# Performance work log

Hardware: AMD Instinct MI355X
Metric: run time of the kernel (lower is better)

## Reference

```python
import jax, jax.numpy as jnp
import numpy as np

EPS = 1e-6
TEMPERATURE = 1.0


def setup_inputs() -> dict:
    key = jax.random.key(0)
    ks = jax.random.split(key, 8)
    B, N, T, H, NH = 128, 16, 32, 128, 4
    L = (N + 1) * T
    node_enc = jax.random.normal(ks[0], (B, T, H), dtype=jnp.float32)
    neigh_enc = jax.random.normal(ks[1], (B, N, T, H), dtype=jnp.float32)
    attn_mask = jax.random.randint(ks[2], (B, L), 0, 2).astype(bool)
    attn_mask = attn_mask.at[:, 0].set(False)  # ensure no fully-masked row
    w_qs = jax.random.normal(ks[3], (NH, H, H), dtype=jnp.float32) * 0.05
    w_ks = jax.random.normal(ks[4], (NH, H, H), dtype=jnp.float32) * 0.05
    w_vs = jax.random.normal(ks[5], (NH, H, H), dtype=jnp.float32) * 0.05
    prj_w = jax.random.normal(ks[6], (H, NH * H), dtype=jnp.float32) * 0.05
    prj_b = jnp.zeros((H,), dtype=jnp.float32)
    ln_gamma = jnp.ones((H,), dtype=jnp.float32)
    ln_beta = jnp.zeros((H,), dtype=jnp.float32)
    return {"node_enc": node_enc, "neigh_enc": neigh_enc, "attn_mask": attn_mask,
            "current_time_step": 5, "w_qs": w_qs, "w_ks": w_ks, "w_vs": w_vs,
            "prj_w": prj_w, "prj_b": prj_b, "ln_gamma": ln_gamma, "ln_beta": ln_beta}


def reference(node_enc, neigh_enc, attn_mask, current_time_step,
              w_qs, w_ks, w_vs, prj_w, prj_b, ln_gamma, ln_beta):
    B, T, H = node_enc.shape
    N = neigh_enc.shape[1]
    NH = w_qs.shape[0]
    q = node_enc[:, current_time_step]                       # [B, H]
    # split(neigh_enc,1,dim=1) + cat(dim=2) == reshape to [B, N*T, H]
    kv = jnp.concatenate([node_enc, neigh_enc.reshape(B, N * T, H)], axis=1)  # [B, L, H]
    q_s = jnp.einsum('bh,nhd->nbd', q, w_qs)                 # [NH, B, H]
    k_s = jnp.einsum('blh,nhd->nbld', kv, w_ks)              # [NH, B, L, H]
    v_s = jnp.einsum('blh,nhd->nbld', kv, w_vs)              # [NH, B, L, H]
    S = jnp.einsum('nbd,nbld->nbl', q_s, k_s)                # [NH, B, L]
    S = jnp.where(attn_mask[None, :, :], -jnp.inf, S)
    S = S / (TEMPERATURE * jnp.sqrt(jnp.float32(H)))
    A = jax.nn.softmax(S, axis=-1)                           # [NH, B, L]
    ctx = jnp.einsum('nbl,nbld->nbd', A, v_s)                # [NH, B, H]
    # torch cat of head-splits along dim=-1 -> [B, NH*H], head-major
    cat = jnp.transpose(ctx, (1, 0, 2)).reshape(B, NH * H)
    proj = cat @ prj_w.T + prj_b                             # [B, H]
    x = proj + q
    mean = jnp.mean(x, axis=-1, keepdims=True)
    var = jnp.var(x, axis=-1, keepdims=True)
    out = (x - mean) / jnp.sqrt(var + EPS) * ln_gamma + ln_beta
    slf_attn = jnp.sum(A, axis=0)[:, None, :]                # [B, 1, L]
    return (out, slf_attn)
```

## Files before the change

kernel.cpp:

```cpp
#include <hip/hip_runtime.h>

#define B_  128
#define N_  16
#define T_  32
#define H_  128
#define NH_ 4
#define L_  544
#define CH  64
#define NC  9

__global__ __launch_bounds__(256) void qk_kernel(
    const float* __restrict__ node_enc, const int* __restrict__ cts_p,
    const float* __restrict__ w_qs, const float* __restrict__ w_ks,
    float* __restrict__ qk_ws)
{
    const int blk = blockIdx.x;
    const int b = blk & 127, n = blk >> 7;
    const int t = threadIdx.x;
    __shared__ float q_sh[H_];
    __shared__ float ps[256];
    __shared__ float qs_sh[H_];

    if (t < H_) q_sh[t] = node_enc[(size_t)b*T_*H_ + cts_p[0]*H_ + t];
    __syncthreads();
    {
        int d = t & 127, half = t >> 7;
        const float* w  = w_qs + (size_t)n*H_*H_ + (half*64)*H_ + d;
        const float* qh = q_sh + half*64;
        float acc = 0.f;
        #pragma unroll 8
        for (int h = 0; h < 64; ++h) acc += qh[h] * w[h*H_];
        ps[t] = acc;
    }
    __syncthreads();
    if (t < H_) qs_sh[t] = ps[t] + ps[t+128];
    __syncthreads();
    {
        int h = t & 127, half = t >> 7;
        const float4* w  = (const float4*)(w_ks + (size_t)n*H_*H_ + h*H_ + half*64);
        const float4* qs = (const float4*)(qs_sh + half*64);
        float acc = 0.f;
        #pragma unroll
        for (int i = 0; i < 16; ++i) {
            float4 wv = w[i], qv = qs[i];
            acc += wv.x*qv.x + wv.y*qv.y + wv.z*qv.z + wv.w*qv.w;
        }
        ps[t] = acc;
    }
    __syncthreads();
    if (t < H_) qk_ws[(b*NH_ + n)*H_ + t] = ps[t] + ps[t+128];
}

__global__ __launch_bounds__(256) void attn_main_kernel(
    const float* __restrict__ node_enc, const float* __restrict__ neigh_enc,
    const int* __restrict__ attn_mask, const float* __restrict__ qk_ws,
    float* __restrict__ S_ws, float* __restrict__ wpart_ws,
    float* __restrict__ stats_ws)
{
    const int blk = blockIdx.x;
    const int b = blk / NC, c = blk % NC;
    const int t = threadIdx.x;
    const int l0 = c * CH;
    const int R  = min(CH, L_ - l0);

    __shared__ __align__(16) float kv_sh[CH*132];
    __shared__ __align__(16) float qk_sh[4*132];
    __shared__ float S_sh[CH*5];
    __shared__ float P_sh[CH*6];
    __shared__ int   msk_sh[CH];

    for (int j = t; j < 4*H_; j += 256) {
        int g = j >> 7, h = j & 127;
        qk_sh[g*132 + h] = qk_ws[(b*NH_ + g)*H_ + h];
    }
    if (t < R) msk_sh[t] = attn_mask[b*L_ + l0 + t];
    for (int j = t; j < R*32; j += 256) {
        int r = j >> 5, cc = j & 31;
        int l = l0 + r;
        const float* rowp = (l < T_)
            ? node_enc  + (size_t)b*T_*H_ + l*H_
            : neigh_enc + (size_t)b*N_*T_*H_ + (size_t)(l - T_)*H_;
        float4 v = ((const float4*)rowp)[cc];
        *((float4*)(kv_sh + r*132 + cc*4)) = v;
    }
    __syncthreads();

    {
        int r = t >> 2, g = t & 3;
        float S = -INFINITY;
        if (r < R) {
            const float4* kvv = (const float4*)(kv_sh + r*132);
            const float4* qv  = (const float4*)(qk_sh + g*132);
            float acc = 0.f;
            #pragma unroll
            for (int i = 0; i < 32; ++i) {
                float4 a = kvv[i], q = qv[i];
                acc += a.x*q.x + a.y*q.y + a.z*q.z + a.w*q.w;
            }
            S = msk_sh[r] ? -INFINITY : acc * 0.08838834764831845f;
            S_ws[((size_t)b*L_ + l0 + r)*NH_ + g] = S;
        }
        S_sh[r*5 + g] = S;
    }
    __syncthreads();

    {
        int w = t >> 6, lane = t & 63;
        float v = S_sh[lane*5 + w];
        float m = v;
        #pragma unroll
        for (int off = 32; off > 0; off >>= 1) m = fmaxf(m, __shfl_xor(m, off, 64));
        m = fmaxf(m, -1e30f);
        float p = __expf(v - m);
        P_sh[lane*6 + w] = p;
        float s = p;
        #pragma unroll
        for (int off = 32; off > 0; off >>= 1) s += __shfl_xor(s, off, 64);
        if (lane == 0) {
            stats_ws[((b*NC + c)*NH_ + w)*2 + 0] = m;
            stats_ws[((b*NC + c)*NH_ + w)*2 + 1] = s;
        }
    }
    __syncthreads();

    {
        int h = t & 127, gp = t >> 7;
        float acc0 = 0.f, acc1 = 0.f;
        #pragma unroll 4
        for (int r = 0; r < R; ++r) {
            float  kvv = kv_sh[r*132 + h];
            float2 p = *((const float2*)(P_sh + r*6 + gp*2));
            acc0 += p.x * kvv;
            acc1 += p.y * kvv;
        }
        float* wp = wpart_ws + (size_t)(b*NC + c)*NH_*H_;
        wp[(gp*2+0)*H_ + h] = acc0;
        wp[(gp*2+1)*H_ + h] = acc1;
    }
}

__global__ __launch_bounds__(512) void finish_kernel(
    const float* __restrict__ node_enc, const int* __restrict__ cts_p,
    const float* __restrict__ w_vs, const float* __restrict__ prj_w,
    const float* __restrict__ prj_b, const float* __restrict__ ln_gamma,
    const float* __restrict__ ln_beta, const float* __restrict__ S_ws,
    const float* __restrict__ wpart_ws, const float* __restrict__ stats_ws,
    float* __restrict__ d_out)
{
    const int b = blockIdx.x, t = threadIdx.x;
    __shared__ float stats_sh[NC*NH_*2];
    __shared__ float m_sh[NH_], inv_sh[NH_];
    __shared__ float scale_sh[NC*NH_];
    __shared__ __align__(16) float wctx_sh[NH_*H_];
    __shared__ __align__(16) float cat_sh[NH_*H_];
    __shared__ float part_sh[512];
    __shared__ float x_sh[H_];
    __shared__ float st2[2];

    if (t < NC*NH_*2) stats_sh[t] = stats_ws[b*NC*NH_*2 + t];
    __syncthreads();
    if (t < NH_) {
        float m = -INFINITY;
        #pragma unroll
        for (int c = 0; c < NC; ++c) m = fmaxf(m, stats_sh[(c*NH_+t)*2]);
        float s = 0.f;
        #pragma unroll
        for (int c = 0; c < NC; ++c)
            s += stats_sh[(c*NH_+t)*2+1] * __expf(stats_sh[(c*NH_+t)*2] - m);
        m_sh[t] = m;
        inv_sh[t] = 1.0f / s;
    }
    __syncthreads();
    if (t < NC*NH_) {
        int c = t >> 2, n = t & 3;
        scale_sh[t] = __expf(stats_sh[(c*NH_+n)*2] - m_sh[n]) * inv_sh[n];
    }
    __syncthreads();

    {
        float m0 = m_sh[0], m1 = m_sh[1], m2 = m_sh[2], m3 = m_sh[3];
        float i0 = inv_sh[0], i1 = inv_sh[1], i2 = inv_sh[2], i3 = inv_sh[3];
        float* slf = d_out + B_*H_ + b*L_;
        const float4* Sr = (const float4*)(S_ws + (size_t)b*L_*NH_);
        for (int l = t; l < L_; l += 512) {
            float4 s4 = Sr[l];
            slf[l] = __expf(s4.x - m0)*i0 + __expf(s4.y - m1)*i1
                   + __expf(s4.z - m2)*i2 + __expf(s4.w - m3)*i3;
        }
    }
    {
        int n = t >> 7;
        const float* wp = wpart_ws + (size_t)b*NC*NH_*H_;
        float acc = 0.f;
        #pragma unroll
        for (int c = 0; c < NC; ++c)
            acc += wp[c*NH_*H_ + t] * scale_sh[c*NH_ + n];
        wctx_sh[t] = acc;
    }
    __syncthreads();
    {
        int n = t >> 7, d = t & 127;
        const float* w  = w_vs + (size_t)n*H_*H_ + d;
        const float* wc = wctx_sh + n*H_;
        float acc = 0.f;
        #pragma unroll 8
        for (int h = 0; h < H_; ++h) acc += wc[h] * w[h*H_];
        cat_sh[t] = acc;
    }
    __syncthreads();
    {
        int j = t >> 2, q = t & 3;
        const float4* w  = (const float4*)(prj_w + (size_t)j*(NH_*H_) + q*128);
        const float4* cc = (const float4*)(cat_sh + q*128);
        float acc = 0.f;
        #pragma unroll
        for (int i = 0; i < 32; ++i) {
            float4 wv = w[i], cv = cc[i];
            acc += wv.x*cv.x + wv.y*cv.y + wv.z*cv.z + wv.w*cv.w;
        }
        part_sh[t] = acc;
    }
    __syncthreads();
    if (t < H_) {
        float x = part_sh[4*t] + part_sh[4*t+1] + part_sh[4*t+2] + part_sh[4*t+3]
                + prj_b[t] + node_enc[(size_t)b*T_*H_ + cts_p[0]*H_ + t];
        x_sh[t] = x;
    }
    __syncthreads();
    if (t < 64) {
        float v0 = x_sh[t], v1 = x_sh[t+64];
        float s1 = v0 + v1, s2 = v0*v0 + v1*v1;
        #pragma unroll
        for (int off = 32; off > 0; off >>= 1) {
            s1 += __shfl_xor(s1, off, 64);
            s2 += __shfl_xor(s2, off, 64);
        }
        if (t == 0) {
            float mean = s1 / (float)H_;
            float var  = s2 / (float)H_ - mean*mean;
            st2[0] = mean;
            st2[1] = rsqrtf(var + 1e-6f);
        }
    }
    __syncthreads();
    if (t < H_)
        d_out[b*H_ + t] = (x_sh[t] - st2[0]) * st2[1] * ln_gamma[t] + ln_beta[t];
}

extern "C" void kernel_launch(void* const* d_in, const int* in_sizes, int n_in,
                              void* d_out, int out_size, void* d_ws, size_t ws_size,
                              hipStream_t stream) {
    const float* node_enc  = (const float*)d_in[0];
    const float* neigh_enc = (const float*)d_in[1];
    const int*   attn_mask = (const int*)d_in[2];
    const int*   cts       = (const int*)d_in[3];
    const float* w_qs      = (const float*)d_in[4];
    const float* w_ks      = (const float*)d_in[5];
    const float* w_vs      = (const float*)d_in[6];
    const float* prj_w     = (const float*)d_in[7];
    const float* prj_b     = (const float*)d_in[8];
    const float* ln_gamma  = (const float*)d_in[9];
    const float* ln_beta   = (const float*)d_in[10];

    float* qk_ws    = (float*)d_ws;
    float* S_ws     = qk_ws + (size_t)B_*NH_*H_;
    float* wpart_ws = S_ws + (size_t)B_*L_*NH_;
    float* stats_ws = wpart_ws + (size_t)B_*NC*NH_*H_;

    qk_kernel<<<B_*NH_, 256, 0, stream>>>(node_enc, cts, w_qs, w_ks, qk_ws);
    attn_main_kernel<<<B_*NC, 256, 0, stream>>>(node_enc, neigh_enc, attn_mask,
                                                qk_ws, S_ws, wpart_ws, stats_ws);
    finish_kernel<<<B_, 512, 0, stream>>>(node_enc, cts, w_vs, prj_w, prj_b,
                                          ln_gamma, ln_beta, S_ws, wpart_ws,
                                          stats_ws, (float*)d_out);
}
```

Baseline: 129.7 us.

## Store chunk-local softmax probs, split finish kernel into two roles, coalesce projection

The attention kernel now writes chunk-local exponentiated probabilities instead of raw scores, so the finish kernel rescales them by per-chunk factors instead of recomputing four exps per position. The finish kernel launches two blocks per batch: one writes the summed attention map, the other does the context, value and projection path plus layernorm. The output projection is rewritten so each wavefront reads contiguous prj_w rows and reduces with shuffles, giving coalesced loads. A launch-bounds occupancy hint is added to the main kernel. The cost is duplicated stats loading in both role blocks.

```diff
diff --git a/kernel.cpp b/kernel.cpp
--- a/kernel.cpp
+++ b/kernel.cpp
@@ -51,10 +51,10 @@
     if (t < H_) qk_ws[(b*NH_ + n)*H_ + t] = ps[t] + ps[t+128];
 }
 
-__global__ __launch_bounds__(256) void attn_main_kernel(
+__global__ __launch_bounds__(256, 4) void attn_main_kernel(
     const float* __restrict__ node_enc, const float* __restrict__ neigh_enc,
     const int* __restrict__ attn_mask, const float* __restrict__ qk_ws,
-    float* __restrict__ S_ws, float* __restrict__ wpart_ws,
+    float* __restrict__ P_ws, float* __restrict__ wpart_ws,
     float* __restrict__ stats_ws)
 {
     const int blk = blockIdx.x;
@@ -98,7 +98,6 @@
                 acc += a.x*q.x + a.y*q.y + a.z*q.z + a.w*q.w;
             }
             S = msk_sh[r] ? -INFINITY : acc * 0.08838834764831845f;
-            S_ws[((size_t)b*L_ + l0 + r)*NH_ + g] = S;
         }
         S_sh[r*5 + g] = S;
     }
@@ -122,6 +121,11 @@
         }
     }
     __syncthreads();
+
+    for (int j = t; j < R*NH_; j += 256) {
+        int r = j >> 2, g = j & 3;
+        P_ws[((size_t)b*L_ + l0 + r)*NH_ + g] = P_sh[r*6 + g];
+    }
 
     {
         int h = t & 127, gp = t >> 7;
@@ -143,19 +147,15 @@
     const float* __restrict__ node_enc, const int* __restrict__ cts_p,
     const float* __restrict__ w_vs, const float* __restrict__ prj_w,
     const float* __restrict__ prj_b, const float* __restrict__ ln_gamma,
-    const float* __restrict__ ln_beta, const float* __restrict__ S_ws,
+    const float* __restrict__ ln_beta, const float* __restrict__ P_ws,
     const float* __restrict__ wpart_ws, const float* __restrict__ stats_ws,
     float* __restrict__ d_out)
 {
-    const int b = blockIdx.x, t = threadIdx.x;
+    const int b = blockIdx.x >> 1, role = blockIdx.x & 1;
+    const int t = threadIdx.x;
     __shared__ float stats_sh[NC*NH_*2];
     __shared__ float m_sh[NH_], inv_sh[NH_];
     __shared__ float scale_sh[NC*NH_];
-    __shared__ __align__(16) float wctx_sh[NH_*H_];
-    __shared__ __align__(16) float cat_sh[NH_*H_];
-    __shared__ float part_sh[512];
-    __shared__ float x_sh[H_];
-    __shared__ float st2[2];
 
     if (t < NC*NH_*2) stats_sh[t] = stats_ws[b*NC*NH_*2 + t];
     __syncthreads();
@@ -177,17 +177,25 @@
     }
     __syncthreads();
 
-    {
-        float m0 = m_sh[0], m1 = m_sh[1], m2 = m_sh[2], m3 = m_sh[3];
-        float i0 = inv_sh[0], i1 = inv_sh[1], i2 = inv_sh[2], i3 = inv_sh[3];
+    if (role == 0) {
         float* slf = d_out + B_*H_ + b*L_;
-        const float4* Sr = (const float4*)(S_ws + (size_t)b*L_*NH_);
+        const float4* Pr = (const float4*)(P_ws + (size_t)b*L_*NH_);
         for (int l = t; l < L_; l += 512) {
-            float4 s4 = Sr[l];
-            slf[l] = __expf(s4.x - m0)*i0 + __expf(s4.y - m1)*i1
-                   + __expf(s4.z - m2)*i2 + __expf(s4.w - m3)*i3;
-        }
-    }
+            float4 p4 = Pr[l];
+            const float* sc = scale_sh + (l >> 6)*NH_;
+            slf[l] = p4.x*sc[0] + p4.y*sc[1] + p4.z*sc[2] + p4.w*sc[3];
+        }
+        return;
+    }
+
+    __shared__ __align__(16) float wctx_sh[NH_*H_];
+    __shared__ __align__(16) float cat_sh[NH_*H_];
+    __shared__ float rb_sh[H_];
+    __shared__ float x_sh[H_];
+    __shared__ float st2[2];
+
+    if (t < H_)
+        rb_sh[t] = prj_b[t] + node_enc[(size_t)b*T_*H_ + cts_p[0]*H_ + t];
     {
         int n = t >> 7;
         const float* wp = wpart_ws + (size_t)b*NC*NH_*H_;
@@ -209,22 +217,20 @@
     }
     __syncthreads();
     {
-        int j = t >> 2, q = t & 3;
-        const float4* w  = (const float4*)(prj_w + (size_t)j*(NH_*H_) + q*128);
-        const float4* cc = (const float4*)(cat_sh + q*128);
-        float acc = 0.f;
-        #pragma unroll
-        for (int i = 0; i < 32; ++i) {
-            float4 wv = w[i], cv = cc[i];
-            acc += wv.x*cv.x + wv.y*cv.y + wv.z*cv.z + wv.w*cv.w;
-        }
-        part_sh[t] = acc;
-    }
-    __syncthreads();
-    if (t < H_) {
-        float x = part_sh[4*t] + part_sh[4*t+1] + part_sh[4*t+2] + part_sh[4*t+3]
-                + prj_b[t] + node_enc[(size_t)b*T_*H_ + cts_p[0]*H_ + t];
-        x_sh[t] = x;
+        int w = t >> 6, lane = t & 63;
+        float4 ca = *((const float4*)(cat_sh + lane*8));
+        float4 cb = *((const float4*)(cat_sh + lane*8 + 4));
+        #pragma unroll
+        for (int i = 0; i < 16; ++i) {
+            int j = w*16 + i;
+            const float4* wr = (const float4*)(prj_w + (size_t)j*(NH_*H_) + lane*8);
+            float4 w0 = wr[0], w1 = wr[1];
+            float d = w0.x*ca.x + w0.y*ca.y + w0.z*ca.z + w0.w*ca.w
+                    + w1.x*cb.x + w1.y*cb.y + w1.z*cb.z + w1.w*cb.w;
+            #pragma unroll
+            for (int off = 32; off > 0; off >>= 1) d += __shfl_xor(d, off, 64);
+            if (lane == 0) x_sh[j] = d + rb_sh[j];
+        }
     }
     __syncthreads();
     if (t < 64) {
@@ -263,14 +269,14 @@
     const float* ln_beta   = (const float*)d_in[10];
 
     float* qk_ws    = (float*)d_ws;
-    float* S_ws     = qk_ws + (size_t)B_*NH_*H_;
-    float* wpart_ws = S_ws + (size_t)B_*L_*NH_;
+    float* P_ws     = qk_ws + (size_t)B_*NH_*H_;
+    float* wpart_ws = P_ws + (size_t)B_*L_*NH_;
     float* stats_ws = wpart_ws + (size_t)B_*NC*NH_*H_;
 
     qk_kernel<<<B_*NH_, 256, 0, stream>>>(node_enc, cts, w_qs, w_ks, qk_ws);
     attn_main_kernel<<<B_*NC, 256, 0, stream>>>(node_enc, neigh_enc, attn_mask,
-                                                qk_ws, S_ws, wpart_ws, stats_ws);
-    finish_kernel<<<B_, 512, 0, stream>>>(node_enc, cts, w_vs, prj_w, prj_b,
-                                          ln_gamma, ln_beta, S_ws, wpart_ws,
-                                          stats_ws, (float*)d_out);
-}
+                                                qk_ws, P_ws, wpart_ws, stats_ws);
+    finish_kernel<<<B_*2, 512, 0, stream>>>(node_enc, cts, w_vs, prj_w, prj_b,
+                                            ln_gamma, ln_beta, P_ws, wpart_ws,
+                                            stats_ws, (float*)d_out);
+}
```

New measurement: 130.2 us. About the same (+0.4%).
